# Performance work log

Measured on AMD Instinct MI355X. Metric: run time of the kernel, lower is better.

## Reference

```python
import jax, jax.numpy as jnp
import numpy as np

N, E, ET = 20000, 200000, 40000
D_IN, H, NEA, HL, OUT = 8, 128, 7, 128, 4
HC = H * NEA  # 896


def _init(k, shape, fan_in):
    return jax.random.normal(k, shape, jnp.float32) * (1.0 / np.sqrt(fan_in))


def setup_inputs() -> dict:
    key = jax.random.key(0)
    ks = list(jax.random.split(key, 16))
    return {
        "x": jax.random.normal(ks[0], (N, D_IN), jnp.float32),
        "edge_index": jax.random.randint(ks[1], (2, E), 0, N),
        "edge_attr": jax.random.uniform(ks[2], (E, NEA), jnp.float32),
        "edge_index_test": jax.random.randint(ks[3], (2, ET), 0, N),
        "W0": _init(ks[4], (NEA, D_IN, H), D_IN), "b0": jnp.zeros((NEA, H), jnp.float32),
        "W1": _init(ks[5], (HC, H), HC), "b1": jnp.zeros((H,), jnp.float32),
        "W2": _init(ks[6], (NEA, H, H), H), "b2": jnp.zeros((NEA, H), jnp.float32),
        "W3": _init(ks[7], (NEA, HC, H), HC), "b3": jnp.zeros((NEA, H), jnp.float32),
        "ew1": _init(ks[8], (NEA, NEA * 4), NEA), "eb1": jnp.zeros((NEA * 4,), jnp.float32),
        "ew2": _init(ks[9], (NEA * 4, NEA * 4), NEA * 4), "eb2": jnp.zeros((NEA * 4,), jnp.float32),
        "ew3": _init(ks[10], (NEA * 4, 1), NEA * 4), "eb3": jnp.zeros((1,), jnp.float32),
        "lw0": _init(ks[11], (2 * HC, HL), 2 * HC), "lb0": jnp.zeros((HL,), jnp.float32),
        "lwh": _init(ks[12], (3, HL, HL), HL), "lbh": jnp.zeros((3, HL), jnp.float32),
        "lw4": _init(ks[13], (HL, OUT), HL), "lb4": jnp.zeros((OUT,), jnp.float32),
    }


def _forward(x, edge_attr, W0, b0, W1, b1, W2, b2, W3, b3,
             ew1, eb1, ew2, eb2, ew3, eb3,
             lw0, lb0, lwh, lbh, lw4, lb4,
             edge_index, edge_index_test):
    n = x.shape[0]
    row, col = edge_index[0], edge_index[1]
    loop = jnp.arange(n)
    # PyG gcn_norm: append self-loops with weight 1
    rows = jnp.concatenate([row, loop])
    cols = jnp.concatenate([col, loop])

    def gcn_norm(w):
        w2 = jnp.concatenate([w, jnp.ones((n,), w.dtype)])
        deg = jax.ops.segment_sum(w2, cols, num_segments=n)
        dis = jnp.where(deg > 0, 1.0 / jnp.sqrt(deg), 0.0)
        return dis[rows] * w2 * dis[cols]  # [E+N]

    norms = [gcn_norm(edge_attr[:, i]) for i in range(NEA)]

    def conv(h, W, b, norm):
        m = (h @ W)[rows] * norm[:, None]  # [E+N, H] gathered messages
        return jax.ops.segment_sum(m, cols, num_segments=n) + b

    x1 = jax.nn.relu(jnp.concatenate([conv(x, W0[i], b0[i], norms[i]) for i in range(NEA)], -1))
    # multi_edge_to_one (edge_fc_layers[1]) -> scalar edge weight in (0,1)
    t = jax.nn.relu(edge_attr @ ew1 + eb1)
    t = jax.nn.relu(t @ ew2 + eb2)
    ew = jax.nn.sigmoid((t @ ew3 + eb3)[:, 0])
    x2 = jax.nn.relu(conv(x1, W1, b1, gcn_norm(ew)))
    x3 = jax.nn.relu(jnp.concatenate([conv(x2, W2[i], b2[i], norms[i]) for i in range(NEA)], -1))
    x4 = jax.nn.relu(jnp.concatenate([conv(x3, W3[i], b3[i], norms[i]) for i in range(NEA)], -1))
    # dropout(p=0.5) is identity in eval mode

    def link_mlp(e):
        h = jax.nn.relu(e @ lw0 + lb0)
        for i in range(3):
            h = jax.nn.relu(h @ lwh[i] + lbh[i])
        return h @ lw4 + lb4

    s, d = edge_index_test[0], edge_index_test[1]
    t1 = link_mlp(jnp.concatenate([x4[s], x4[d]], -1))
    t2 = link_mlp(jnp.concatenate([x4[d], x4[s]], -1))[:, jnp.array([0, 2, 1, 3])]
    return 0.5 * (t1 + t2)  # [E_test, 4]


def reference(x, edge_index, edge_attr, edge_index_test,
              W0, b0, W1, b1, W2, b2, W3, b3,
              ew1, eb1, ew2, eb2, ew3, eb3,
              lw0, lb0, lwh, lbh, lw4, lb4):
    return _forward(x, edge_attr, W0, b0, W1, b1, W2, b2, W3, b3,
                    ew1, eb1, ew2, eb2, ew3, eb3,
                    lw0, lb0, lwh, lbh, lw4, lb4,
                    edge_index, edge_index_test)
```

## Files before the change

kernel.cpp:

```cpp
#include <hip/hip_runtime.h>
#include <math.h>

#define NN 20000
#define NE 200000
#define NT 40000
#define HP 136

typedef _Float16 f16;
typedef __attribute__((ext_vector_type(8))) _Float16 f16x8;
typedef __attribute__((ext_vector_type(4))) float f32x4;
typedef __attribute__((ext_vector_type(2))) _Float16 h2;

__global__ void k_edge_mlp(const float* __restrict__ ea,
                           const float* __restrict__ w1, const float* __restrict__ b1,
                           const float* __restrict__ w2, const float* __restrict__ b2,
                           const float* __restrict__ w3, const float* __restrict__ b3,
                           const int* __restrict__ col,
                           float* __restrict__ out, int* __restrict__ cnt) {
  int e = blockIdx.x * 256 + threadIdx.x;
  if (e >= NE) return;
  atomicAdd(&cnt[col[e]], 1);
  float a[7];
#pragma unroll
  for (int i = 0; i < 7; i++) a[i] = ea[e * 7 + i];
  float t1[28];
#pragma unroll
  for (int j = 0; j < 28; j++) {
    float s = b1[j];
#pragma unroll
    for (int k = 0; k < 7; k++) s = fmaf(a[k], w1[k * 28 + j], s);
    t1[j] = fmaxf(s, 0.f);
  }
  float t2[28];
  for (int j = 0; j < 28; j++) {
    float s = b2[j];
    for (int k = 0; k < 28; k++) s = fmaf(t1[k], w2[k * 28 + j], s);
    t2[j] = fmaxf(s, 0.f);
  }
  float s = b3[0];
  for (int k = 0; k < 28; k++) s = fmaf(t2[k], w3[k], s);
  out[e] = 1.f / (1.f + expf(-s));
}

__global__ void k_scan(int* __restrict__ cnt, int* __restrict__ rowptr) {
  __shared__ int sums[256];
  __shared__ int offs[256];
  int t = threadIdx.x;
  const int CH = (NN + 255) / 256;
  int base = t * CH;
  int s = 0;
  for (int i = 0; i < CH; i++) { int idx = base + i; if (idx < NN) s += cnt[idx]; }
  sums[t] = s;
  __syncthreads();
  if (t == 0) {
    int acc = 0;
    for (int i = 0; i < 256; i++) { offs[i] = acc; acc += sums[i]; }
    rowptr[NN] = acc;
  }
  __syncthreads();
  int acc = offs[t];
  for (int i = 0; i < CH; i++) {
    int idx = base + i;
    if (idx < NN) {
      int cv = cnt[idx];
      rowptr[idx] = acc;
      cnt[idx] = acc;
      acc += cv;
    }
  }
}

__global__ void k_fill_csr(const int* __restrict__ col, int* __restrict__ cursor,
                           int* __restrict__ eid) {
  int e = blockIdx.x * 256 + threadIdx.x;
  if (e >= NE) return;
  int pos = atomicAdd(&cursor[col[e]], 1);
  eid[pos] = e;
}

__global__ __launch_bounds__(64) void k_deg_csr(const int* __restrict__ rowptr,
                                                const int* __restrict__ eid,
                                                const float* __restrict__ ea,
                                                const float* __restrict__ ewb,
                                                float* __restrict__ dis) {
  int t = threadIdx.x;
  int n = blockIdx.x * 8 + (t >> 3);
  int i = t & 7;
  if (n >= NN) return;
  float deg = 1.f;
  int s = rowptr[n], e2 = rowptr[n + 1];
  for (int p = s; p < e2; p++) {
    int e = eid[p];
    deg += (i < 7) ? ea[e * 7 + i] : ewb[e];
  }
  dis[i * NN + n] = rsqrtf(deg);
}

__global__ void k_csr_norms(const int* __restrict__ eid, const int* __restrict__ row,
                            const int* __restrict__ col, const float* __restrict__ ea,
                            const float* __restrict__ ew, const float* __restrict__ dis,
                            int* __restrict__ csr_src, float* __restrict__ csr_norm) {
  int p = blockIdx.x * 256 + threadIdx.x;
  if (p >= NE) return;
  int e = eid[p];
  int r = row[e], c = col[e];
  csr_src[p] = r;
#pragma unroll
  for (int i = 0; i < 7; i++)
    csr_norm[i * NE + p] = dis[i * NN + r] * ea[e * 7 + i] * dis[i * NN + c];
  csr_norm[7 * NE + p] = dis[7 * NN + r] * ew[e] * dis[7 * NN + c];
}

__global__ void k_wprep_all(const float* __restrict__ W1, const float* __restrict__ W2,
                            const float* __restrict__ W3, const float* __restrict__ lw0,
                            const float* __restrict__ lwh,
                            f16* __restrict__ w1t, f16* __restrict__ w2t,
                            f16* __restrict__ w3t, f16* __restrict__ lw0t,
                            f16* __restrict__ lwht, int* __restrict__ cursor) {
  int b = blockIdx.x, t = threadIdx.x;
  const float* W;
  f16* D;
  int K, g, tile;
  size_t matOff;
  if (b < 448) {
    W = W1; D = w1t; K = 896; g = 0; tile = b; matOff = 0;
  } else if (b < 896) {
    int l = b - 448; W = W2; D = w2t; K = 128; g = l >> 6; tile = l & 63;
    matOff = 16384;
  } else if (b < 4032) {
    int l = b - 896; W = W3; D = w3t; K = 896; g = l / 448; tile = l % 448;
    matOff = 114688;
  } else if (b < 4928) {
    int l = b - 4032; W = lw0; D = lw0t; K = 896; g = l / 448; tile = l % 448;
    matOff = 114688;
  } else if (b < 5120) {
    int l = b - 4928; W = lwh; D = lwht; K = 128; g = l >> 6; tile = l & 63;
    matOff = 16384;
  } else {
    int idx = (b - 5120) * 256 + t;
    if (idx < NN) cursor[idx] = 0;
    return;
  }
  int idx = tile * 256 + t;
  int k = idx >> 7, n = idx & 127;
  float v = W[(size_t)g * matOff + (size_t)k * 128 + n];
  D[(size_t)g * 128 * K + (size_t)n * K + k] = (f16)v;
}

template <int OUTM, bool RELU, bool BIAS, bool GROUP_A, bool SWIZZLE>
__global__ __launch_bounds__(256) void k_mgemm(
    const f16* __restrict__ A, const f16* __restrict__ BT,
    const float* __restrict__ bias,
    float* __restrict__ Cf, f16* __restrict__ Ch,
    int ldA, int M, int K, int NG, int GXp) {
  int rowT, g;
  if (SWIZZLE) {
    int b = blockIdx.x;
    int xcd = b & 7, s = b >> 3;
    g = s % NG;
    int lr = s / NG;
    rowT = lr * 8 + xcd;
    if (rowT >= GXp) return;
  } else {
    rowT = blockIdx.x;
    g = blockIdx.y;
  }
  __shared__ f16 smem[8192];
  const int tid = threadIdx.x;
  const int w = tid >> 6, lane = tid & 63;
  const int quad = lane >> 4, lc = lane & 15;
  const int wr = w >> 1, wc = w & 1;
  const int bm = rowT * 128;
  const int ldC = NG * 128;
  const int cb = g * 128;
  const int aoff = GROUP_A ? g * K : 0;
  const f16* Bg = BT + (size_t)g * 128 * K;
  const int srow = lane >> 2, skoff = (lane & 3) * 8;

  f32x4 acc[4][4] = {};

  for (int k0 = 0; k0 < K; k0 += 32) {
#pragma unroll
    for (int l = 0; l < 4; l++) {
      int c = w + l * 4;
      int t = c >> 3, r16 = c & 7;
      int rowi = r16 * 16 + srow;
      f16* ldst = smem + t * 4096 + r16 * 512;
      const f16* src;
      if (t == 0) {
        int gm = bm + rowi;
        if (gm > M - 1) gm = M - 1;
        src = A + (size_t)gm * ldA + aoff + k0 + skoff;
      } else {
        src = Bg + (size_t)rowi * K + k0 + skoff;
      }
      __builtin_amdgcn_global_load_lds(
          (const __attribute__((address_space(1))) void*)src,
          (__attribute__((address_space(3))) void*)ldst, 16, 0, 0);
    }
    __syncthreads();
    f16x8 bf[4];
#pragma unroll
    for (int nt = 0; nt < 4; nt++) {
      int r = wc * 64 + nt * 16 + lc;
      bf[nt] = *(const f16x8*)(smem + 4096 + r * 32 + quad * 8);
    }
#pragma unroll
    for (int mt = 0; mt < 4; mt++) {
      int r = wr * 64 + mt * 16 + lc;
      f16x8 ah = *(const f16x8*)(smem + r * 32 + quad * 8);
#pragma unroll
      for (int nt = 0; nt < 4; nt++) {
        acc[mt][nt] = __builtin_amdgcn_mfma_f32_16x16x32_f16(ah, bf[nt], acc[mt][nt], 0, 0, 0);
      }
    }
    __syncthreads();
  }

  float bv[4];
  if (BIAS) {
#pragma unroll
    for (int nt = 0; nt < 4; nt++) bv[nt] = bias[cb + wc * 64 + nt * 16 + lc];
  }
#pragma unroll
  for (int mt = 0; mt < 4; mt++) {
#pragma unroll
    for (int r = 0; r < 4; r++) {
      int gm = bm + wr * 64 + mt * 16 + quad * 4 + r;
      if (gm >= M) continue;
#pragma unroll
      for (int nt = 0; nt < 4; nt++) {
        float v = acc[mt][nt][r];
        if (BIAS) v += bv[nt];
        if (RELU) v = fmaxf(v, 0.f);
        size_t idx = (size_t)gm * ldC + cb + wc * 64 + nt * 16 + lc;
        if (OUTM == 1) Ch[idx] = (f16)v;
        else Cf[idx] = v;
      }
    }
  }
}

__global__ __launch_bounds__(448) void k_agg7(const f16* __restrict__ hW,
                                              const float* __restrict__ csr_norm,
                                              const float* __restrict__ dis,
                                              const int* __restrict__ rowptr,
                                              const int* __restrict__ csr_src,
                                              const float* __restrict__ bias,
                                              f16* __restrict__ outq) {
  int n = blockIdx.x;
  int f2 = threadIdx.x;
  int i = f2 >> 6;
  const h2* hw2 = (const h2*)hW;
  const float* nrm = csr_norm + (size_t)i * NE;
  float d = dis[i * NN + n];
  h2 sv = hw2[(size_t)n * 448 + f2];
  float ax = d * d * (float)sv.x, ay = d * d * (float)sv.y;
  int s = rowptr[n], e = rowptr[n + 1];
  int p = s;
  for (; p + 8 <= e; p += 8) {
    int si[8];
    float nn_[8];
    h2 vv[8];
#pragma unroll
    for (int u = 0; u < 8; u++) { si[u] = csr_src[p + u]; nn_[u] = nrm[p + u]; }
#pragma unroll
    for (int u = 0; u < 8; u++) vv[u] = hw2[(size_t)si[u] * 448 + f2];
#pragma unroll
    for (int u = 0; u < 8; u++) {
      ax = fmaf(nn_[u], (float)vv[u].x, ax);
      ay = fmaf(nn_[u], (float)vv[u].y, ay);
    }
  }
  for (; p + 4 <= e; p += 4) {
    int s0 = csr_src[p], s1 = csr_src[p + 1], s2 = csr_src[p + 2], s3 = csr_src[p + 3];
    float n0 = nrm[p], n1 = nrm[p + 1], n2 = nrm[p + 2], n3 = nrm[p + 3];
    h2 v0 = hw2[(size_t)s0 * 448 + f2];
    h2 v1 = hw2[(size_t)s1 * 448 + f2];
    h2 v2 = hw2[(size_t)s2 * 448 + f2];
    h2 v3 = hw2[(size_t)s3 * 448 + f2];
    ax = fmaf(n0, (float)v0.x, ax); ay = fmaf(n0, (float)v0.y, ay);
    ax = fmaf(n1, (float)v1.x, ax); ay = fmaf(n1, (float)v1.y, ay);
    ax = fmaf(n2, (float)v2.x, ax); ay = fmaf(n2, (float)v2.y, ay);
    ax = fmaf(n3, (float)v3.x, ax); ay = fmaf(n3, (float)v3.y, ay);
  }
  for (; p < e; p++) {
    int s0 = csr_src[p];
    float n0 = nrm[p];
    h2 v0 = hw2[(size_t)s0 * 448 + f2];
    ax = fmaf(n0, (float)v0.x, ax); ay = fmaf(n0, (float)v0.y, ay);
  }
  h2 o;
  o.x = (f16)fmaxf(ax + bias[2 * f2], 0.f);
  o.y = (f16)fmaxf(ay + bias[2 * f2 + 1], 0.f);
  ((h2*)outq)[(size_t)n * 448 + f2] = o;
}

__global__ __launch_bounds__(256) void k_agg1(const f16* __restrict__ hW,
                                              const float* __restrict__ nrm,
                                              const float* __restrict__ dis_i,
                                              const int* __restrict__ rowptr,
                                              const int* __restrict__ csr_src,
                                              const float* __restrict__ bias,
                                              f16* __restrict__ x2h) {
  int t = threadIdx.x;
  int n = blockIdx.x * 4 + (t >> 6);
  int f2 = t & 63;
  if (n >= NN) return;
  const h2* hw2 = (const h2*)hW;
  float d = dis_i[n];
  h2 sv = hw2[(size_t)n * 64 + f2];
  float ax = d * d * (float)sv.x, ay = d * d * (float)sv.y;
  int s = rowptr[n], e = rowptr[n + 1];
  int p = s;
  for (; p + 8 <= e; p += 8) {
    int si[8];
    float nn_[8];
    h2 vv[8];
#pragma unroll
    for (int u = 0; u < 8; u++) { si[u] = csr_src[p + u]; nn_[u] = nrm[p + u]; }
#pragma unroll
    for (int u = 0; u < 8; u++) vv[u] = hw2[(size_t)si[u] * 64 + f2];
#pragma unroll
    for (int u = 0; u < 8; u++) {
      ax = fmaf(nn_[u], (float)vv[u].x, ax);
      ay = fmaf(nn_[u], (float)vv[u].y, ay);
    }
  }
  for (; p < e; p++) {
    int s0 = csr_src[p];
    float n0 = nrm[p];
    h2 v0 = hw2[(size_t)s0 * 64 + f2];
    ax = fmaf(n0, (float)v0.x, ax); ay = fmaf(n0, (float)v0.y, ay);
  }
  h2 o;
  o.x = (f16)fmaxf(ax + bias[2 * f2], 0.f);
  o.y = (f16)fmaxf(ay + bias[2 * f2 + 1], 0.f);
  ((h2*)x2h)[(size_t)n * 64 + f2] = o;
}

__global__ __launch_bounds__(256) void k_agg2(const f16* __restrict__ x2h,
                                              const float* __restrict__ csr_norm,
                                              const float* __restrict__ dis,
                                              const int* __restrict__ rowptr,
                                              const int* __restrict__ csr_src,
                                              f16* __restrict__ oq) {
  int t = threadIdx.x;
  int n = blockIdx.x * 4 + (t >> 6);
  int f2 = t & 63;
  if (n >= NN) return;
  const h2* x2 = (const h2*)x2h;
  h2 svh = x2[(size_t)n * 64 + f2];
  float svx = (float)svh.x, svy = (float)svh.y;
  float ax[7], ay[7];
#pragma unroll
  for (int i = 0; i < 7; i++) {
    float d = dis[i * NN + n];
    ax[i] = d * d * svx;
    ay[i] = d * d * svy;
  }
  int s = rowptr[n], e = rowptr[n + 1];
  int p = s;
  for (; p + 4 <= e; p += 4) {
    int si[4];
    h2 vv[4];
#pragma unroll
    for (int u = 0; u < 4; u++) si[u] = csr_src[p + u];
#pragma unroll
    for (int u = 0; u < 4; u++) vv[u] = x2[(size_t)si[u] * 64 + f2];
#pragma unroll
    for (int i = 0; i < 7; i++) {
#pragma unroll
      for (int u = 0; u < 4; u++) {
        float nw = csr_norm[(size_t)i * NE + p + u];
        ax[i] = fmaf(nw, (float)vv[u].x, ax[i]);
        ay[i] = fmaf(nw, (float)vv[u].y, ay[i]);
      }
    }
  }
  for (; p < e; p++) {
    int s0 = csr_src[p];
    h2 v0 = x2[(size_t)s0 * 64 + f2];
#pragma unroll
    for (int i = 0; i < 7; i++) {
      float nw = csr_norm[(size_t)i * NE + p];
      ax[i] = fmaf(nw, (float)v0.x, ax[i]);
      ay[i] = fmaf(nw, (float)v0.y, ay[i]);
    }
  }
#pragma unroll
  for (int i = 0; i < 7; i++) {
    h2 o;
    o.x = (f16)ax[i];
    o.y = (f16)ay[i];
    ((h2*)oq)[(size_t)n * 448 + i * 64 + f2] = o;
  }
}

__global__ __launch_bounds__(64) void k_agg_x(const float* __restrict__ x,
                                              const float* __restrict__ csr_norm,
                                              const float* __restrict__ dis,
                                              const int* __restrict__ rowptr,
                                              const int* __restrict__ csr_src,
                                              float* __restrict__ xagg) {
  int n = blockIdx.x;
  int f = threadIdx.x;
  if (f >= 56) return;
  int i = f >> 3, c = f & 7;
  float d = dis[i * NN + n];
  float acc = d * d * x[(size_t)n * 8 + c];
  int s = rowptr[n], e = rowptr[n + 1];
  for (int p = s; p < e; p++)
    acc = fmaf(csr_norm[i * NE + p], x[(size_t)csr_src[p] * 8 + c], acc);
  xagg[(size_t)n * 56 + f] = acc;
}

__global__ __launch_bounds__(896) void k_gemm0(const float* __restrict__ xagg,
                                               const float* __restrict__ W0,
                                               const float* __restrict__ b0,
                                               f16* __restrict__ outq) {
  int n = blockIdx.x;
  int f = threadIdx.x;
  int i = f >> 7, h = f & 127;
  float s = b0[i * 128 + h];
#pragma unroll
  for (int c = 0; c < 8; c++)
    s = fmaf(xagg[(size_t)n * 56 + i * 8 + c], W0[(i * 8 + c) * 128 + h], s);
  outq[(size_t)n * 896 + f] = (f16)fmaxf(s, 0.f);
}

__global__ __launch_bounds__(256) void k_link_fused(
    const float* __restrict__ UV, const int* __restrict__ eit,
    const float* __restrict__ lb0, const f16* __restrict__ lwht,
    const float* __restrict__ lbh, const float* __restrict__ lw4,
    const float* __restrict__ lb4, float* __restrict__ out) {
  __shared__ f16 Hhi[64 * HP];
  __shared__ f16 Hlo[64 * HP];
  __shared__ f16 Wt[128 * HP];
  __shared__ float ob[64][4];
  const int tid = threadIdx.x;
  const int t0 = blockIdx.x * 32;
  {
    int c = tid & 127;
    int rbase = tid >> 7;
    for (int it = 0; it < 32; it++) {
      int rr = rbase + it * 2;
      int tp = t0 + (rr >> 1), dir = rr & 1;
      int s = eit[tp], d = eit[NT + tp];
      int a = dir ? d : s, b = dir ? s : d;
      float v = UV[(size_t)a * 256 + c] + UV[(size_t)b * 256 + 128 + c] + lb0[c];
      v = fmaxf(v, 0.f);
      f16 h = (f16)v;
      Hhi[rr * HP + c] = h;
      Hlo[rr * HP + c] = (f16)(v - (float)h);
    }
  }
  const int w = tid >> 6, lane = tid & 63;
  const int quad = lane >> 4, lc = lane & 15;
  for (int l = 0; l < 3; l++) {
    __syncthreads();
    {
      const f16* src = lwht + (size_t)l * 128 * 128;
#pragma unroll
      for (int it = 0; it < 8; it++) {
        int idx = (tid + it * 256) * 8;
        int n = idx >> 7, k = idx & 127;
        *(float4*)&Wt[n * HP + k] = *(const float4*)&src[idx];
      }
    }
    __syncthreads();
    f32x4 acc[8] = {};
    const int arow = w * 16 + lc;
#pragma unroll
    for (int k0 = 0; k0 < 128; k0 += 32) {
      f16x8 ah = *(const f16x8*)&Hhi[arow * HP + k0 + quad * 8];
      f16x8 al = *(const f16x8*)&Hlo[arow * HP + k0 + quad * 8];
#pragma unroll
      for (int nt = 0; nt < 8; nt++) {
        f16x8 bf = *(const f16x8*)&Wt[(nt * 16 + lc) * HP + k0 + quad * 8];
        acc[nt] = __builtin_amdgcn_mfma_f32_16x16x32_f16(ah, bf, acc[nt], 0, 0, 0);
        acc[nt] = __builtin_amdgcn_mfma_f32_16x16x32_f16(al, bf, acc[nt], 0, 0, 0);
      }
    }
#pragma unroll
    for (int nt = 0; nt < 8; nt++) {
      int col = nt * 16 + lc;
      float bb = lbh[l * 128 + col];
#pragma unroll
      for (int r = 0; r < 4; r++) {
        int rrow = w * 16 + quad * 4 + r;
        float v = fmaxf(acc[nt][r] + bb, 0.f);
        f16 h = (f16)v;
        Hhi[rrow * HP + col] = h;
        Hlo[rrow * HP + col] = (f16)(v - (float)h);
      }
    }
  }
  __syncthreads();
  {
    int rr = tid >> 2, j = tid & 3;
    float o = lb4[j];
    for (int k = 0; k < 128; k++) {
      float hv = (float)Hhi[rr * HP + k] + (float)Hlo[rr * HP + k];
      o = fmaf(hv, lw4[k * 4 + j], o);
    }
    ob[rr][j] = o;
  }
  __syncthreads();
  if (tid < 128) {
    int tp = tid >> 2, j = tid & 3;
    const int perm[4] = {0, 2, 1, 3};
    out[(size_t)(t0 + tp) * 4 + j] = 0.5f * (ob[2 * tp][j] + ob[2 * tp + 1][perm[j]]);
  }
}

extern "C" void kernel_launch(void* const* d_in, const int* in_sizes, int n_in,
                              void* d_out, int out_size, void* d_ws, size_t ws_size,
                              hipStream_t stream) {
  const float* x   = (const float*)d_in[0];
  const int*   ei  = (const int*)d_in[1];
  const float* ea  = (const float*)d_in[2];
  const int*   eit = (const int*)d_in[3];
  const float* W0  = (const float*)d_in[4];
  const float* b0  = (const float*)d_in[5];
  const float* W1  = (const float*)d_in[6];
  const float* b1  = (const float*)d_in[7];
  const float* W2  = (const float*)d_in[8];
  const float* b2  = (const float*)d_in[9];
  const float* W3  = (const float*)d_in[10];
  const float* b3  = (const float*)d_in[11];
  const float* ew1 = (const float*)d_in[12];
  const float* eb1 = (const float*)d_in[13];
  const float* ew2 = (const float*)d_in[14];
  const float* eb2 = (const float*)d_in[15];
  const float* ew3 = (const float*)d_in[16];
  const float* eb3 = (const float*)d_in[17];
  const float* lw0 = (const float*)d_in[18];
  const float* lb0 = (const float*)d_in[19];
  const float* lwh = (const float*)d_in[20];
  const float* lbh = (const float*)d_in[21];
  const float* lw4 = (const float*)d_in[22];
  const float* lb4 = (const float*)d_in[23];
  const int* row = ei;
  const int* col = ei + NE;
  float* out = (float*)d_out;

  char* ws = (char*)d_ws;
  size_t off = 0;
  auto alloc = [&](size_t bytes) -> char* {
    char* p = ws + off;
    off += (bytes + 255) & ~(size_t)255;
    return p;
  };
  f16*   xA     = (f16*)alloc((size_t)NN * 896 * 2);
  f16*   xB     = (f16*)alloc((size_t)NN * 896 * 2);
  f16*   x2h    = (f16*)alloc((size_t)NN * 128 * 2);
  float* UV     = (float*)alloc((size_t)NN * 256 * 4);
  float* csr_nrm= (float*)alloc((size_t)8 * NE * 4);
  float* dis    = (float*)alloc((size_t)8 * NN * 4);
  float* ewb    = (float*)alloc((size_t)NE * 4);
  int*   rowptr = (int*)alloc((size_t)(NN + 1) * 4);
  int*   cursor = (int*)alloc((size_t)NN * 4);
  int*   eid    = (int*)alloc((size_t)NE * 4);
  int*   csr_src= (int*)alloc((size_t)NE * 4);
  f16* w1t  = (f16*)alloc((size_t)128 * 896 * 2);
  f16* w2t  = (f16*)alloc((size_t)7 * 128 * 128 * 2);
  f16* w3t  = (f16*)alloc((size_t)7 * 128 * 896 * 2);
  f16* lw0t = (f16*)alloc((size_t)2 * 128 * 896 * 2);
  f16* lwht = (f16*)alloc((size_t)3 * 128 * 128 * 2);
  float* xagg = UV;
  (void)ws_size; (void)in_sizes; (void)n_in; (void)out_size;

  const int EB = (NE + 255) / 256;
  const int GX = (NN + 127) / 128;
  const int MC = (GX + 7) / 8;

  k_wprep_all<<<5120 + (NN + 255) / 256, 256, 0, stream>>>(
      W1, W2, W3, lw0, lwh, w1t, w2t, w3t, lw0t, lwht, cursor);

  k_edge_mlp<<<EB, 256, 0, stream>>>(ea, ew1, eb1, ew2, eb2, ew3, eb3, col, ewb, cursor);
  k_scan<<<1, 256, 0, stream>>>(cursor, rowptr);
  k_fill_csr<<<EB, 256, 0, stream>>>(col, cursor, eid);
  k_deg_csr<<<(NN + 7) / 8, 64, 0, stream>>>(rowptr, eid, ea, ewb, dis);
  k_csr_norms<<<EB, 256, 0, stream>>>(eid, row, col, ea, ewb, dis, csr_src, csr_nrm);

  k_agg_x<<<NN, 64, 0, stream>>>(x, csr_nrm, dis, rowptr, csr_src, xagg);
  k_gemm0<<<NN, 896, 0, stream>>>(xagg, W0, b0, xA);

  k_mgemm<1, false, false, false, false><<<dim3(GX, 1), 256, 0, stream>>>(
      xA, w1t, nullptr, nullptr, xB, 896, NN, 896, 1, GX);
  k_agg1<<<(NN + 3) / 4, 256, 0, stream>>>(xB, csr_nrm + (size_t)7 * NE,
                                           dis + (size_t)7 * NN, rowptr, csr_src, b1, x2h);

  k_agg2<<<(NN + 3) / 4, 256, 0, stream>>>(x2h, csr_nrm, dis, rowptr, csr_src, xB);
  k_mgemm<1, true, true, true, false><<<dim3(GX, 7), 256, 0, stream>>>(
      xB, w2t, b2, nullptr, xA, 896, NN, 128, 7, GX);

  k_mgemm<1, false, false, false, true><<<dim3(8 * MC * 7), 256, 0, stream>>>(
      xA, w3t, nullptr, nullptr, xB, 896, NN, 896, 7, GX);
  k_agg7<<<NN, 448, 0, stream>>>(xB, csr_nrm, dis, rowptr, csr_src, b3, xA);

  k_mgemm<0, false, false, false, true><<<dim3(8 * MC * 2), 256, 0, stream>>>(
      xA, lw0t, nullptr, UV, nullptr, 896, NN, 896, 2, GX);

  k_link_fused<<<NT / 32, 256, 0, stream>>>(UV, eit, lb0, lwht, lbh, lw4, lb4, out);
}
```

Before: 577.2 us.

## Remap agg7 blocks per channel across XCDs and store UV in fp16

The 7-channel aggregation kernel now runs 256-thread blocks that each cover 4 nodes of a single channel. The block index is mapped so each XCD works on one channel's normalization array and feature slice, which should improve L2 locality of the gathered rows. The link-layer UV intermediate is written and read as fp16 instead of fp32, halving that traffic at some cost in precision. xagg gets its own buffer instead of aliasing UV.

```diff
diff --git a/kernel.cpp b/kernel.cpp
--- a/kernel.cpp
+++ b/kernel.cpp
@@ -241,23 +241,30 @@
   }
 }
 
-__global__ __launch_bounds__(448) void k_agg7(const f16* __restrict__ hW,
+__global__ __launch_bounds__(256) void k_agg7(const f16* __restrict__ hW,
                                               const float* __restrict__ csr_norm,
                                               const float* __restrict__ dis,
                                               const int* __restrict__ rowptr,
                                               const int* __restrict__ csr_src,
                                               const float* __restrict__ bias,
                                               f16* __restrict__ outq) {
-  int n = blockIdx.x;
-  int f2 = threadIdx.x;
-  int i = f2 >> 6;
+  int b = blockIdx.x;
+  int xcd = b & 7, s = b >> 3;
+  int i, chunk;
+  if (xcd < 7) { i = xcd; chunk = s; }
+  else { i = s / 625; chunk = 4375 + s % 625; }
+  int t = threadIdx.x;
+  int n = chunk * 4 + (t >> 6);
+  int f2 = t & 63;
+  if (n >= NN) return;
   const h2* hw2 = (const h2*)hW;
   const float* nrm = csr_norm + (size_t)i * NE;
+  const int base = i * 64 + f2;
   float d = dis[i * NN + n];
-  h2 sv = hw2[(size_t)n * 448 + f2];
+  h2 sv = hw2[(size_t)n * 448 + base];
   float ax = d * d * (float)sv.x, ay = d * d * (float)sv.y;
-  int s = rowptr[n], e = rowptr[n + 1];
-  int p = s;
+  int st = rowptr[n], e = rowptr[n + 1];
+  int p = st;
   for (; p + 8 <= e; p += 8) {
     int si[8];
     float nn_[8];
@@ -265,35 +272,23 @@
 #pragma unroll
     for (int u = 0; u < 8; u++) { si[u] = csr_src[p + u]; nn_[u] = nrm[p + u]; }
 #pragma unroll
-    for (int u = 0; u < 8; u++) vv[u] = hw2[(size_t)si[u] * 448 + f2];
+    for (int u = 0; u < 8; u++) vv[u] = hw2[(size_t)si[u] * 448 + base];
 #pragma unroll
     for (int u = 0; u < 8; u++) {
       ax = fmaf(nn_[u], (float)vv[u].x, ax);
       ay = fmaf(nn_[u], (float)vv[u].y, ay);
     }
   }
-  for (; p + 4 <= e; p += 4) {
-    int s0 = csr_src[p], s1 = csr_src[p + 1], s2 = csr_src[p + 2], s3 = csr_src[p + 3];
-    float n0 = nrm[p], n1 = nrm[p + 1], n2 = nrm[p + 2], n3 = nrm[p + 3];
-    h2 v0 = hw2[(size_t)s0 * 448 + f2];
-    h2 v1 = hw2[(size_t)s1 * 448 + f2];
-    h2 v2 = hw2[(size_t)s2 * 448 + f2];
-    h2 v3 = hw2[(size_t)s3 * 448 + f2];
-    ax = fmaf(n0, (float)v0.x, ax); ay = fmaf(n0, (float)v0.y, ay);
-    ax = fmaf(n1, (float)v1.x, ax); ay = fmaf(n1, (float)v1.y, ay);
-    ax = fmaf(n2, (float)v2.x, ax); ay = fmaf(n2, (float)v2.y, ay);
-    ax = fmaf(n3, (float)v3.x, ax); ay = fmaf(n3, (float)v3.y, ay);
-  }
   for (; p < e; p++) {
     int s0 = csr_src[p];
     float n0 = nrm[p];
-    h2 v0 = hw2[(size_t)s0 * 448 + f2];
+    h2 v0 = hw2[(size_t)s0 * 448 + base];
     ax = fmaf(n0, (float)v0.x, ax); ay = fmaf(n0, (float)v0.y, ay);
   }
   h2 o;
-  o.x = (f16)fmaxf(ax + bias[2 * f2], 0.f);
-  o.y = (f16)fmaxf(ay + bias[2 * f2 + 1], 0.f);
-  ((h2*)outq)[(size_t)n * 448 + f2] = o;
+  o.x = (f16)fmaxf(ax + bias[i * 128 + 2 * f2], 0.f);
+  o.y = (f16)fmaxf(ay + bias[i * 128 + 2 * f2 + 1], 0.f);
+  ((h2*)outq)[(size_t)n * 448 + base] = o;
 }
 
 __global__ __launch_bounds__(256) void k_agg1(const f16* __restrict__ hW,
@@ -430,7 +425,7 @@
 }
 
 __global__ __launch_bounds__(256) void k_link_fused(
-    const float* __restrict__ UV, const int* __restrict__ eit,
+    const f16* __restrict__ UV, const int* __restrict__ eit,
     const float* __restrict__ lb0, const f16* __restrict__ lwht,
     const float* __restrict__ lbh, const float* __restrict__ lw4,
     const float* __restrict__ lb4, float* __restrict__ out) {
@@ -448,7 +443,8 @@
       int tp = t0 + (rr >> 1), dir = rr & 1;
       int s = eit[tp], d = eit[NT + tp];
       int a = dir ? d : s, b = dir ? s : d;
-      float v = UV[(size_t)a * 256 + c] + UV[(size_t)b * 256 + 128 + c] + lb0[c];
+      float v = (float)UV[(size_t)a * 256 + c] + (float)UV[(size_t)b * 256 + 128 + c]
+                + lb0[c];
       v = fmaxf(v, 0.f);
       f16 h = (f16)v;
       Hhi[rr * HP + c] = h;
@@ -555,7 +551,8 @@
   f16*   xA     = (f16*)alloc((size_t)NN * 896 * 2);
   f16*   xB     = (f16*)alloc((size_t)NN * 896 * 2);
   f16*   x2h    = (f16*)alloc((size_t)NN * 128 * 2);
-  float* UV     = (float*)alloc((size_t)NN * 256 * 4);
+  f16*   UVh    = (f16*)alloc((size_t)NN * 256 * 2);
+  float* xagg   = (float*)alloc((size_t)NN * 56 * 4);
   float* csr_nrm= (float*)alloc((size_t)8 * NE * 4);
   float* dis    = (float*)alloc((size_t)8 * NN * 4);
   float* ewb    = (float*)alloc((size_t)NE * 4);
@@ -568,7 +565,6 @@
   f16* w3t  = (f16*)alloc((size_t)7 * 128 * 896 * 2);
   f16* lw0t = (f16*)alloc((size_t)2 * 128 * 896 * 2);
   f16* lwht = (f16*)alloc((size_t)3 * 128 * 128 * 2);
-  float* xagg = UV;
   (void)ws_size; (void)in_sizes; (void)n_in; (void)out_size;
 
   const int EB = (NE + 255) / 256;
@@ -598,10 +594,10 @@
 
   k_mgemm<1, false, false, false, true><<<dim3(8 * MC * 7), 256, 0, stream>>>(
       xA, w3t, nullptr, nullptr, xB, 896, NN, 896, 7, GX);
-  k_agg7<<<NN, 448, 0, stream>>>(xB, csr_nrm, dis, rowptr, csr_src, b3, xA);
-
-  k_mgemm<0, false, false, false, true><<<dim3(8 * MC * 2), 256, 0, stream>>>(
-      xA, lw0t, nullptr, UV, nullptr, 896, NN, 896, 2, GX);
-
-  k_link_fused<<<NT / 32, 256, 0, stream>>>(UV, eit, lb0, lwht, lbh, lw4, lb4, out);
-}
+  k_agg7<<<8 * 4375, 256, 0, stream>>>(xB, csr_nrm, dis, rowptr, csr_src, b3, xA);
+
+  k_mgemm<1, false, false, false, true><<<dim3(8 * MC * 2), 256, 0, stream>>>(
+      xA, lw0t, nullptr, nullptr, UVh, 896, NN, 896, 2, GX);
+
+  k_link_fused<<<NT / 32, 256, 0, stream>>>(UVh, eit, lb0, lwht, lbh, lw4, lb4, out);
+}
```

New measurement: 586.7 us. About the same (+1.6%).
